# Performance work log

Measured on AMD Instinct MI355X. Metric: run time of the kernel, lower is better.

Reference implementation:

```python
import jax, jax.numpy as jnp
import numpy as np

TOP_K = 2


def setup_inputs() -> dict:
    key = jax.random.key(0)
    k0, k1, k2, k3 = jax.random.split(key, 4)
    N, D, O, E = 131072, 512, 512, 16
    H = D // 4  # gate hidden: gate_input_size // 4
    x = jax.random.normal(k0, (N, D), dtype=jnp.float32)
    # gate MLP params (task_bh=0 gate; Linear weights stored as [in, out])
    Wg1 = jax.random.normal(k1, (D, H), dtype=jnp.float32) / np.sqrt(D).astype(np.float32)
    bg1 = jnp.zeros((H,), jnp.float32)
    Wg2 = jax.random.normal(k2, (H, E), dtype=jnp.float32) * 0.02
    bg2 = jnp.zeros((E,), jnp.float32)
    # per-expert Linear(D, O) weights stacked [E, D, O]
    We = jax.random.normal(k3, (E, D, O), dtype=jnp.float32) / np.sqrt(D).astype(np.float32)
    be = jnp.zeros((E, O), jnp.float32)
    return {"x": x, "Wg1": Wg1, "bg1": bg1, "Wg2": Wg2, "bg2": bg2,
            "We": We, "be": be, "task_bh": 0}


def reference(x, Wg1, bg1, Wg2, bg2, We, be, task_bh):
    # --- top_k_gating (noisy_gating=False path) ---
    h = jax.nn.gelu(x @ Wg1 + bg1, approximate=False)  # nn.GELU default is exact erf
    logits = h @ Wg2 + bg2                              # [N, E]
    probs = jax.nn.softmax(logits, axis=1) + 1e-4       # [N, E]
    top_g, top_i = jax.lax.top_k(probs, TOP_K)          # [N, K]
    N, E = probs.shape
    # dense gate matrix: zeros.scatter(1, top_k_indices, top_k_gates)
    gates = jnp.zeros_like(probs).at[jnp.arange(N)[:, None], top_i].set(top_g)
    # --- dispatch / per-expert GEMM / combine ---
    # Equivalent to: gather tokens per expert, expert Linear, scale by gate,
    # scatter-add back. Since gates[n, e] == 0 for unselected experts, the
    # combined output equals sum_e gates[:, e] * (x @ We[e] + be[e]).
    def body(acc, ewb):
        W_e, b_e, g_e = ewb                      # [D,O], [O], [N]
        return acc + g_e[:, None] * (x @ W_e + b_e), None
    init = jnp.zeros((N, We.shape[2]), x.dtype)
    out, _ = jax.lax.scan(body, init, (We, be, gates.T))
    return out
```

## Files before the change

kernel.cpp:

```cpp
#include <hip/hip_runtime.h>
#include <cstdint>
#include <math.h>


#define NTOK 131072
#define DDIM 512
#define NT 16

typedef _Float16 f16;
typedef f16   f16x8 __attribute__((ext_vector_type(8)));
typedef float f32x4 __attribute__((ext_vector_type(4)));

__device__ __forceinline__ void load_lds16(const void* g, void* l){
  __builtin_amdgcn_global_load_lds(
      (const __attribute__((address_space(1))) void*)(uintptr_t)g,
      (__attribute__((address_space(3))) void*)(uintptr_t)l, 16, 0, 0);
}

__device__ __forceinline__ f32x4 MFMAH(f16x8 a, f16x8 b, f32x4 c){
  return __builtin_amdgcn_mfma_f32_16x16x32_f16(a, b, c, 0, 0, 0);
}

__device__ __forceinline__ f16x8 readF64h(const char* buf, int r, int q){
  return *(const f16x8*)(buf + r*128 + ((q ^ (r & 7)) << 4));
}
__device__ __forceinline__ f16x8 pack8f(const float* fv){
  f16x8 v;
  #pragma unroll
  for (int j=0;j<8;++j) v[j] = (f16)fv[j];
  return v;
}

__global__ void kconv(const float* __restrict__ We, const float* __restrict__ Wg1,
                      const float* __restrict__ Wg2,
                      f16* __restrict__ Wt, f16* __restrict__ W1, char* __restrict__ Wg2f,
                      int* __restrict__ ctrl){
  __shared__ float sh[64*65];
  int bx = blockIdx.x, tid = threadIdx.x;
  if (bx < 1024){
    int e = bx >> 6, dt = (bx >> 3) & 7, ot = bx & 7;
    const float* src = We + (size_t)e*262144 + (size_t)dt*64*512 + ot*64;
    #pragma unroll
    for (int it=0; it<16; ++it){ int idx = it*256+tid; int dl = idx>>6, ol = idx&63;
      sh[dl*65+ol] = src[dl*512+ol]; }
    __syncthreads();
    f16* dst = Wt + (size_t)e*262144 + (size_t)ot*64*512 + dt*64;
    #pragma unroll
    for (int it=0; it<16; ++it){ int idx = it*256+tid; int ol = idx>>6, dl = idx&63;
      dst[(size_t)ol*512+dl] = (f16)sh[dl*65+ol]; }
  } else if (bx < 1040){
    int q = bx - 1024;
    int dt = q >> 1, ht = q & 1;
    const float* src = Wg1 + (size_t)dt*64*128 + ht*64;
    #pragma unroll
    for (int it=0; it<16; ++it){ int idx = it*256+tid; int dl = idx>>6, ol = idx&63;
      sh[dl*65+ol] = src[dl*128+ol]; }
    __syncthreads();
    #pragma unroll
    for (int it=0; it<16; ++it){ int idx = it*256+tid; int ol = idx>>6, dl = idx&63;
      W1[(size_t)(ht*64+ol)*512 + dt*64+dl] = (f16)sh[dl*65+ol]; }
  } else {
    int ks = tid >> 6, l = tid & 63;
    int col = l & 15, kb = ks*32 + ((l >> 4) << 3);
    f16x8 v;
    #pragma unroll
    for (int j=0;j<8;++j) v[j] = (f16)Wg2[(kb+j)*16 + col];
    *(f16x8*)(Wg2f + (ks*64+l)*16) = v;
    #pragma unroll
    for (int i = 0; i < 8; ++i) ctrl[tid + i*256] = 0;
  }
}

__global__ __launch_bounds__(256) void kgate(
    const float* __restrict__ x, const f16* __restrict__ W1, const char* __restrict__ Wg2f,
    const float* __restrict__ bg1, const float* __restrict__ bg2,
    f16* __restrict__ xbf,
    int2* __restrict__ gate_e, float2* __restrict__ gate_g,
    int* __restrict__ refine_cnt, int* __restrict__ refine_list, int* __restrict__ counts)
{
  __shared__ __align__(16) char sm[76800];
  const int BOFF = 32768;
  const int LOGI = 67584;
  const int HIST = 75776;
  int tid = threadIdx.x, bid = blockIdx.x;
  int lane = tid & 63, w = tid >> 6, wm = w >> 1, wn = w & 1;
  int l15 = lane & 15, l4 = lane >> 4;
  int t0 = bid * 128;
  int ar = tid >> 1, ach = tid & 1;
  const float* xrow = x + (size_t)(t0 + ar) * DDIM;
  char* xbfb = (char*)xbf;
  f32x4 acc[4][4];
  #pragma unroll
  for (int n=0;n<4;++n){
    float bb = bg1[wn*64 + n*16 + l15];
    f32x4 z = {bb, bb, bb, bb};
    #pragma unroll
    for (int m=0;m<4;++m) acc[m][n] = z;
  }
  auto stageA = [&](int ks, char* abuf){
    float fv[32];
    #pragma unroll
    for (int q=0;q<8;++q) *(float4*)&fv[q*4] = *(const float4*)(xrow + ks*64 + ach*32 + q*4);
    f16x8 h0 = pack8f(fv), h1 = pack8f(fv+8), h2 = pack8f(fv+16), h3 = pack8f(fv+24);
    *(f16x8*)(abuf + ar*128 + (((ach*4+0) ^ (ar & 7)) << 4)) = h0;
    *(f16x8*)(abuf + ar*128 + (((ach*4+1) ^ (ar & 7)) << 4)) = h1;
    *(f16x8*)(abuf + ar*128 + (((ach*4+2) ^ (ar & 7)) << 4)) = h2;
    *(f16x8*)(abuf + ar*128 + (((ach*4+3) ^ (ar & 7)) << 4)) = h3;
    if (xbf){
      char* xd = xbfb + (size_t)(t0+ar)*1024 + ks*128 + ach*64;
      *(f16x8*)xd = h0; *(f16x8*)(xd+16) = h1; *(f16x8*)(xd+32) = h2; *(f16x8*)(xd+48) = h3;
    }
  };
  auto stageB = [&](int ks, char* lds){
    const char* gb = (const char*)W1 + ks*128;
    #pragma unroll
    for (int i = 0; i < 4; ++i){
      int lin = i*4096 + tid*16;
      int r = lin >> 7, g = (lin >> 4) & 7;
      load_lds16(gb + r*1024 + ((g ^ (r & 7)) << 4), lds + i*4096 + ((tid >> 6) << 10));
    }
  };
  stageB(0, sm + BOFF); stageA(0, sm);
  for (int ks = 0; ks < 8; ++ks){
    int b = ks & 1;
    asm volatile("s_waitcnt vmcnt(0)" ::: "memory");
    __syncthreads();
    if (ks < 7) stageB(ks+1, sm + BOFF + (b^1)*16384);
    const char* Ab = sm + b*16384;
    const char* Bb = sm + BOFF + b*16384;
    f16x8 ah[4][2], bh[4][2];
    #pragma unroll
    for (int m=0;m<4;++m)
      #pragma unroll
      for (int kf=0;kf<2;++kf) ah[m][kf] = readF64h(Ab, wm*64 + m*16 + l15, kf*4 + l4);
    #pragma unroll
    for (int n=0;n<4;++n)
      #pragma unroll
      for (int kf=0;kf<2;++kf) bh[n][kf] = readF64h(Bb, wn*64 + n*16 + l15, kf*4 + l4);
    #pragma unroll
    for (int m=0;m<4;++m)
      #pragma unroll
      for (int n=0;n<4;++n){
        acc[m][n] = MFMAH(ah[m][0], bh[n][0], acc[m][n]);
        acc[m][n] = MFMAH(ah[m][1], bh[n][1], acc[m][n]);
      }
    if (ks < 7) stageA(ks+1, sm + (b^1)*16384);
  }
  __syncthreads();
  uint4 wgf[4];
  #pragma unroll
  for (int ksq=0; ksq<4; ++ksq) wgf[ksq] = *(const uint4*)(Wg2f + (ksq*64+lane)*16);
  float* hl = (float*)sm;
  #pragma unroll
  for (int m=0;m<4;++m)
    #pragma unroll
    for (int n=0;n<4;++n)
      #pragma unroll
      for (int j=0;j<4;++j){
        int row = wm*64 + m*16 + (l4 << 2) + j;
        int col = wn*64 + n*16 + l15;
        float uv = acc[m][n][j];
        hl[row*132 + col] = 0.5f * uv * (1.0f + erff(uv * 0.70710678118654752f));
      }
  __syncthreads();
  {
    float bb2 = bg2[l15];
    float* ll = (float*)(sm + LOGI);
    #pragma unroll
    for (int sub=0; sub<2; ++sub){
      f32x4 acc2 = {bb2, bb2, bb2, bb2};
      #pragma unroll
      for (int ksq=0; ksq<4; ++ksq){
        const float* hp = (const float*)sm + (w*32 + sub*16 + l15)*132 + ksq*32 + l4*8;
        f16x8 afr;
        #pragma unroll
        for (int j=0;j<8;++j) afr[j] = (f16)hp[j];
        acc2 = MFMAH(afr, *(const f16x8*)&wgf[ksq], acc2);
      }
      #pragma unroll
      for (int j=0;j<4;++j) ll[(w*32 + sub*16 + l4*4 + j)*16 + l15] = acc2[j];
    }
  }
  int* hist = (int*)(sm + HIST);
  hist[tid] = 0;
  __syncthreads();
  if (tid < 128){
    int t = t0 + tid;
    const float* l = (const float*)(sm + LOGI) + tid*16;
    float b1 = -1e30f, b2 = -1e30f, b3 = -1e30f; int e1 = 0, e2 = 0;
    #pragma unroll
    for (int e = 0; e < 16; ++e){
      float v = l[e];
      if (v > b1){ b3 = b2; b2 = b1; e2 = e1; b1 = v; e1 = e; }
      else if (v > b2){ b3 = b2; b2 = v; e2 = e; }
      else if (v > b3){ b3 = v; }
    }
    float s = 0.f;
    #pragma unroll
    for (int e = 0; e < 16; ++e) s += expf(l[e] - b1);
    float inv = 1.f / s;
    gate_e[t] = make_int2(e1, e2);
    gate_g[t] = make_float2(inv + 1e-4f, expf(b2 - b1) * inv + 1e-4f);
    if (b2 - b3 < 1e-3f){
      int pos = atomicAdd(refine_cnt, 1);
      refine_list[pos] = t;
    }
    int pa = min(e1, e2), pb = max(e1, e2);
    atomicAdd(&hist[pa*16 + pb], 1);
  }
  __syncthreads();
  if (hist[tid]) atomicAdd(&counts[tid], hist[tid]);
}

__global__ __launch_bounds__(128) void krefine(
    const float* __restrict__ x, const float* __restrict__ Wg1, const float* __restrict__ bg1,
    const float* __restrict__ Wg2, const float* __restrict__ bg2,
    const int* __restrict__ refine_cnt, const int* __restrict__ refine_list,
    int2* __restrict__ gate_e, float2* __restrict__ gate_g, int* __restrict__ counts)
{
  __shared__ float  xs[512];
  __shared__ double hd[128];
  __shared__ double ld[16];
  int tid = threadIdx.x;
  int rc = *refine_cnt;
  for (int i = blockIdx.x; i < rc; i += gridDim.x){
    __syncthreads();
    int t = refine_list[i];
    *(float4*)(xs + tid*4) = *(const float4*)(x + (size_t)t*DDIM + tid*4);
    __syncthreads();
    double a0=0.0, a1=0.0, a2=0.0, a3=0.0;
    for (int d = 0; d < 512; d += 4){
      a0 += (double)xs[d]   * (double)Wg1[(d)*128 + tid];
      a1 += (double)xs[d+1] * (double)Wg1[(d+1)*128 + tid];
      a2 += (double)xs[d+2] * (double)Wg1[(d+2)*128 + tid];
      a3 += (double)xs[d+3] * (double)Wg1[(d+3)*128 + tid];
    }
    double a = (double)bg1[tid] + ((a0+a1)+(a2+a3));
    hd[tid] = 0.5 * a * (1.0 + erf(a * 0.70710678118654752440));
    __syncthreads();
    if (tid < 16){
      double s0=0.0, s1=0.0;
      for (int k = 0; k < 128; k += 2){
        s0 += hd[k]   * (double)Wg2[(k)*16 + tid];
        s1 += hd[k+1] * (double)Wg2[(k+1)*16 + tid];
      }
      ld[tid] = (double)bg2[tid] + s0 + s1;
    }
    __syncthreads();
    if (tid == 0){
      int2 olde = gate_e[t];
      double b1 = -1e300, b2 = -1e300; int e1 = 0, e2 = 0;
      for (int e = 0; e < 16; ++e){
        double v = ld[e];
        if (v > b1){ b2 = b1; e2 = e1; b1 = v; e1 = e; }
        else if (v > b2){ b2 = v; e2 = e; }
      }
      double s = 0.0;
      for (int e = 0; e < 16; ++e) s += exp(ld[e] - b1);
      double inv = 1.0 / s;
      int oldp = min(olde.x, olde.y)*16 + max(olde.x, olde.y);
      int newp = min(e1, e2)*16 + max(e1, e2);
      if (oldp != newp){ atomicSub(&counts[oldp], 1); atomicAdd(&counts[newp], 1); }
      gate_e[t] = make_int2(e1, e2);
      gate_g[t] = make_float2((float)(inv + 1e-4), (float)(exp(b2 - b1) * inv + 1e-4));
    }
  }
}

__global__ __launch_bounds__(256) void kscatter(
    const int2* __restrict__ gate_e, const float2* __restrict__ gate_g,
    const int* __restrict__ counts,
    int* __restrict__ bases, int* __restrict__ cursors,
    int* __restrict__ tile_pair, int* __restrict__ tile_row0, int* __restrict__ ntiles,
    int* __restrict__ pair_tok, float2* __restrict__ pair_g, int ts)
{
  __shared__ int h[256];
  __shared__ int gb[256];
  __shared__ int bl[257];
  int tid = threadIdx.x;
  h[tid] = 0;
  if (tid < 64){
    int l = tid;
    int4 c = *(const int4*)(counts + l*4);
    int s = c.x + c.y + c.z + c.w;
    int ps = s;
    #pragma unroll
    for (int d = 1; d < 64; d <<= 1){ int v = __shfl_up(ps, d); if (l >= d) ps += v; }
    int ex = ps - s;
    bl[4*l+0] = ex;
    bl[4*l+1] = ex + c.x;
    bl[4*l+2] = ex + c.x + c.y;
    bl[4*l+3] = ex + c.x + c.y + c.z;
    if (l == 63) bl[256] = ex + s;
    if (blockIdx.x == 0){
      *(int4*)(bases + 4*l) = make_int4(bl[4*l], bl[4*l+1], bl[4*l+2], bl[4*l+3]);
      if (l == 63) bases[256] = ex + s;
      int t0 = (c.x + ts-1)/ts, t1 = (c.y + ts-1)/ts, t2 = (c.z + ts-1)/ts, t3 = (c.w + ts-1)/ts;
      int tsum = t0 + t1 + t2 + t3;
      int pt = tsum;
      #pragma unroll
      for (int d = 1; d < 64; d <<= 1){ int v = __shfl_up(pt, d); if (l >= d) pt += v; }
      int ext = pt - tsum;
      if (l == 63) *ntiles = ext + tsum;
      int tb = ext;
      int cc[4] = {c.x, c.y, c.z, c.w};
      #pragma unroll
      for (int j = 0; j < 4; ++j){
        int pp = 4*l + j;
        for (int r = 0; r < cc[j]; r += ts){ tile_pair[tb] = pp; tile_row0[tb] = r; ++tb; }
      }
    }
  }
  __syncthreads();
  int t = blockIdx.x*256 + tid;
  int2 ee = gate_e[t]; float2 gg = gate_g[t];
  int a, b; float ga, gbv;
  if (ee.x < ee.y){ a = ee.x; b = ee.y; ga = gg.x; gbv = gg.y; }
  else            { a = ee.y; b = ee.x; ga = gg.y; gbv = gg.x; }
  int p = a*16 + b;
  int off = atomicAdd(&h[p], 1);
  __syncthreads();
  if (h[tid]) gb[tid] = bl[tid] + atomicAdd(&cursors[tid], h[tid]);
  __syncthreads();
  int slot = gb[p] + off;
  pair_tok[slot] = t;
  pair_g[slot] = make_float2(ga, gbv);
}

#define SB0 __builtin_amdgcn_sched_barrier(0)
#define PH_MID do{ __builtin_amdgcn_s_barrier(); \
                   asm volatile("s_waitcnt lgkmcnt(0)"); SB0; }while(0)
#define PH_END do{ SB0; __builtin_amdgcn_s_barrier(); }while(0)

#define RDA(hp, mb) do{ \
  _Pragma("unroll") for (int m_=0;m_<4;++m_){ \
    int r_ = ((mb)+m_)*16 + l15; \
    af[m_][0] = readF64h(hp, r_, l4); \
    af[m_][1] = readF64h(hp, r_, 4+l4); }}while(0)
#define RDB(hp, bv, nb) do{ \
  _Pragma("unroll") for (int n_=0;n_<2;++n_){ \
    int r_ = bln + ((nb)+n_)*16 + l15; \
    bv[n_][0] = readF64h(hp, r_, l4); \
    bv[n_][1] = readF64h(hp, r_, 4+l4); }}while(0)
#define MMAC(bv, mb, nb) do{ \
  __builtin_amdgcn_s_setprio(1); \
  _Pragma("unroll") for (int m_=0;m_<4;++m_){ \
    _Pragma("unroll") for (int n_=0;n_<2;++n_){ \
      acc[(mb)+m_][(nb)+n_] = MFMAH(af[m_][0], bv[n_][0], acc[(mb)+m_][(nb)+n_]); \
      acc[(mb)+m_][(nb)+n_] = MFMAH(af[m_][1], bv[n_][1], acc[(mb)+m_][(nb)+n_]); }} \
  __builtin_amdgcn_s_setprio(0); \
}while(0)

__global__ __launch_bounds__(512, 2) void kexpert2(
    const f16* __restrict__ xbf, const f16* __restrict__ Wt, const float* __restrict__ be,
    float* __restrict__ out,
    const int* __restrict__ counts, const int* __restrict__ bases,
    const int* __restrict__ tile_pair, const int* __restrict__ tile_row0, const int* __restrict__ ntiles,
    const int* __restrict__ pair_tok, const float2* __restrict__ pair_g)
{
  __shared__ __align__(16) char sm[134144];
  const int BBASE = 65536, LTOK = 131072, LG = 132096;
  int bid = blockIdx.x;
  int tile = ((bid >> 4) << 3) | (bid & 7);
  int nt = (bid >> 3) & 1;
  if (tile >= *ntiles) return;
  int p = tile_pair[tile], row0 = tile_row0[tile];
  int base = bases[p], cnt = counts[p];
  int eA = p >> 4, eB = p & 15;
  int tid = threadIdx.x, lane = tid & 63, w = tid >> 6;
  int wm = w >> 2, wn = w & 3;
  int l15 = lane & 15, l4 = lane >> 4;
  int bln = (wn & 1) * 64;
  if (tid < 256){
    int rr = row0 + tid; bool v = rr < cnt;
    ((int*)(sm + LTOK))[tid] = v ? pair_tok[base + rr] : -1;
    ((float2*)(sm + LG))[tid] = v ? pair_g[base + rr] : make_float2(0.f, 1.f);
  }
  __syncthreads();

  int rr0 = tid >> 3;
  int sw = ((tid & 7) ^ (rr0 & 7)) << 4;
  const char* xb = (const char*)xbf;
  const char* srcA[2][2];
  #pragma unroll
  for (int h = 0; h < 2; ++h)
    #pragma unroll
    for (int i = 0; i < 2; ++i){
      int tk = ((const int*)(sm + LTOK))[h*128 + i*64 + rr0];
      if (tk < 0) tk = 0;
      srcA[h][i] = xb + (size_t)tk*1024 + sw;
    }
  const char* srcB0 = (const char*)Wt + (size_t)eA*524288 + (size_t)(nt*256 + rr0)*1024 + sw;
  long long edelt = ((long long)eB - eA) * 524288;
  char* dA = sm + w*1024;
  char* dB = sm + BBASE + w*1024;

  auto stA = [&](int t, int h){
    if (t >= NT) return;
    int ks = t & 7, bf_ = t & 1;
    load_lds16(srcA[h][0] + ks*128, dA + bf_*32768 + h*16384);
    load_lds16(srcA[h][1] + ks*128, dA + bf_*32768 + h*16384 + 8192);
  };
  auto stB = [&](int t, int h){
    if (t >= NT) return;
    int ks = t & 7, bf_ = t & 1;
    long long eo = ((t >= 8) ? edelt : 0) + ks*128;
    load_lds16(srcB0 + h*131072 + eo,         dB + bf_*32768 + h*16384);
    load_lds16(srcB0 + h*131072 + 65536 + eo, dB + bf_*32768 + h*16384 + 8192);
  };

  const char* A0 = sm + wm*16384;
  const char* A1 = A0 + 32768;
  const char* B0 = sm + BBASE + (wn >> 1)*16384;
  const char* B1 = B0 + 32768;

  f32x4 acc[8][4];
  #pragma unroll
  for (int m = 0; m < 8; ++m)
    #pragma unroll
    for (int n = 0; n < 4; ++n) acc[m][n] = (f32x4){0.f,0.f,0.f,0.f};

  stA(0,0); stA(0,1); stB(0,0); stB(0,1); stB(1,0); stB(1,1);
  asm volatile("s_waitcnt vmcnt(4)"); SB0;
  __builtin_amdgcn_s_barrier();

  f16x8 af[4][2], bL[2][2], bH[2][2];
  #pragma unroll 1
  for (int i = 0; i < 8; ++i){
    int t0 = 2*i, t1 = t0 + 1;
    RDA(A0, 0); RDB(B0, bL, 0); stA(t1, 0);
    PH_MID; MMAC(bL, 0, 0); PH_END;
    RDB(B0, bH, 2); stA(t1, 1);
    PH_MID; MMAC(bH, 0, 2); PH_END;
    RDA(A0, 4); stB(t0+2, 0);
    PH_MID; MMAC(bH, 4, 2); PH_END;
    stB(t0+2, 1);
    if (i != 7) { asm volatile("s_waitcnt vmcnt(4)"); SB0; }
    else        { asm volatile("s_waitcnt vmcnt(0)"); SB0; }
    PH_MID; MMAC(bL, 4, 0); PH_END;
    RDA(A1, 0); RDB(B1, bL, 0); stA(t0+2, 0);
    PH_MID; MMAC(bL, 0, 0); PH_END;
    RDB(B1, bH, 2); stA(t0+2, 1);
    PH_MID; MMAC(bH, 0, 2); PH_END;
    RDA(A1, 4); stB(t1+2, 0);
    PH_MID; MMAC(bH, 4, 2); PH_END;
    stB(t1+2, 1);
    if (i != 7) { asm volatile("s_waitcnt vmcnt(4)"); SB0; }
    PH_MID; MMAC(bL, 4, 0); PH_END;
    if (i == 3){
      #pragma unroll
      for (int m = 0; m < 8; ++m)
        #pragma unroll
        for (int j = 0; j < 4; ++j){
          int row = wm*128 + m*16 + l4*4 + j;
          float2 g2 = ((const float2*)(sm + LG))[row];
          float r_ = g2.x / g2.y;
          #pragma unroll
          for (int n = 0; n < 4; ++n) acc[m][n][j] *= r_;
        }
    }
  }

  float bcA[4], bcB[4];
  #pragma unroll
  for (int n = 0; n < 4; ++n){
    int col = nt*256 + wn*64 + n*16 + l15;
    bcA[n] = be[(size_t)eA*DDIM + col];
    bcB[n] = be[(size_t)eB*DDIM + col];
  }
  #pragma unroll
  for (int m = 0; m < 8; ++m)
    #pragma unroll
    for (int j = 0; j < 4; ++j){
      int row = wm*128 + m*16 + l4*4 + j;
      int tk = ((const int*)(sm + LTOK))[row];
      if (tk >= 0){
        float2 g2 = ((const float2*)(sm + LG))[row];
        float* orow = out + (size_t)tk*DDIM + nt*256 + wn*64;
        #pragma unroll
        for (int n = 0; n < 4; ++n)
          orow[n*16 + l15] = g2.y*acc[m][n][j] + g2.x*bcA[n] + g2.y*bcB[n];
      }
    }
}

__global__ __launch_bounds__(256, 2) void kexpertF(
    const float* __restrict__ x,
    const f16* __restrict__ Wt, const float* __restrict__ be,
    float* __restrict__ out,
    const int* __restrict__ counts, const int* __restrict__ bases,
    const int* __restrict__ tile_pair, const int* __restrict__ tile_row0, const int* __restrict__ ntiles,
    const int* __restrict__ pair_tok, const float2* __restrict__ pair_g)
{
  __shared__ __align__(16) char sm[67072];
  const int ABUF = 0, BBUF = 32768, LTOK = 65536, LGOFF = 66048;
  int tile = blockIdx.x >> 2, nt = blockIdx.x & 3;
  if (tile >= *ntiles) return;
  int p = tile_pair[tile], row0 = tile_row0[tile];
  int base = bases[p], cnt = counts[p];
  int eA = p >> 4, eB = p & 15;
  int tid = threadIdx.x, lane = tid & 63;
  int w = tid >> 6, wm = w >> 1, wn = w & 1;
  if (tid < 128){
    int rr = row0 + tid; bool v = rr < cnt;
    ((int*)(sm + LTOK))[tid] = v ? pair_tok[base + rr] : -1;
    ((float2*)(sm + LGOFF))[tid] = v ? pair_g[base + rr] : make_float2(0.f, 0.f);
  }
  __syncthreads();
  const char* wb = (const char*)Wt;
  int grp = tid >> 3, gch = tid & 7;
  int swz = (gch ^ (grp & 7)) << 4;
  long long edelt = ((long long)eB - (long long)eA) * 524288;
  const char* srcB[4];
  #pragma unroll
  for (int i = 0; i < 4; ++i)
    srcB[i] = wb + (long long)eA*524288 + (size_t)(nt*128 + i*32 + grp)*1024 + swz;
  int arow = tid >> 1, ach = tid & 1;
  int tkr = ((const int*)(sm + LTOK))[arow];
  if (tkr < 0) tkr = 0;
  const float* xrow = x + (size_t)tkr*DDIM + ach*32;
  int ldst = (w << 10);
  #pragma unroll
  for (int i = 0; i < 4; ++i) load_lds16(srcB[i], sm + BBUF + i*4096 + ldst);
  {
    #pragma unroll
    for (int q2 = 0; q2 < 4; ++q2){
      float fv[8];
      *(float4*)&fv[0] = *(const float4*)(xrow + q2*8);
      *(float4*)&fv[4] = *(const float4*)(xrow + q2*8 + 4);
      f16x8 hv = pack8f(fv);
      int g = ach*4 + q2;
      *(f16x8*)(sm + ABUF + arow*128 + ((g ^ (arow & 7)) << 4)) = hv;
    }
  }
  f32x4 acc[4][4], res[4][4];
  #pragma unroll
  for (int m=0;m<4;++m)
    #pragma unroll
    for (int n=0;n<4;++n) acc[m][n] = (f32x4){0.f,0.f,0.f,0.f};
  for (int u = 0; u < 16; ++u){
    int b = u & 1;
    asm volatile("s_waitcnt vmcnt(0)" ::: "memory");
    __syncthreads();
    int un = u + 1;
    f16x8 hv[4];
    if (un < 16){
      int b2 = un & 1;
      long long aoff = (long long)(un & 7) * 128;
      long long boff = aoff + ((un >> 3) ? edelt : 0);
      #pragma unroll
      for (int i = 0; i < 4; ++i)
        load_lds16(srcB[i] + boff, sm + BBUF + b2*16384 + i*4096 + ldst);
      const float* xr = xrow + (un & 7)*64;
      #pragma unroll
      for (int q2 = 0; q2 < 4; ++q2){
        float fv[8];
        *(float4*)&fv[0] = *(const float4*)(xr + q2*8);
        *(float4*)&fv[4] = *(const float4*)(xr + q2*8 + 4);
        hv[q2] = pack8f(fv);
      }
    }
    const char* Ab = sm + ABUF + b*16384;
    const char* Bb = sm + BBUF + b*16384;
    f16x8 af2[4][2], bf2[4][2];
    #pragma unroll
    for (int m=0;m<4;++m){
      int r = wm*64 + m*16 + (lane & 15);
      af2[m][0] = readF64h(Ab, r, (lane >> 4));
      af2[m][1] = readF64h(Ab, r, 4 + (lane >> 4));
    }
    #pragma unroll
    for (int n=0;n<4;++n){
      int r = wn*64 + n*16 + (lane & 15);
      bf2[n][0] = readF64h(Bb, r, (lane >> 4));
      bf2[n][1] = readF64h(Bb, r, 4 + (lane >> 4));
    }
    #pragma unroll
    for (int m=0;m<4;++m)
      #pragma unroll
      for (int n=0;n<4;++n){
        acc[m][n] = MFMAH(af2[m][0], bf2[n][0], acc[m][n]);
        acc[m][n] = MFMAH(af2[m][1], bf2[n][1], acc[m][n]);
      }
    if (un < 16){
      int b2 = un & 1;
      #pragma unroll
      for (int q2 = 0; q2 < 4; ++q2){
        int g = ach*4 + q2;
        *(f16x8*)(sm + ABUF + b2*16384 + arow*128 + ((g ^ (arow & 7)) << 4)) = hv[q2];
      }
    }
    if (u == 7){
      const float* bev = be + (size_t)eA*DDIM + nt*128;
      float bcol[4];
      #pragma unroll
      for (int n=0;n<4;++n) bcol[n] = bev[wn*64 + n*16 + (lane & 15)];
      #pragma unroll
      for (int m=0;m<4;++m)
        #pragma unroll
        for (int j=0;j<4;++j){
          int row = wm*64 + m*16 + ((lane >> 4) << 2) + j;
          float g = ((const float2*)(sm + LGOFF))[row].x;
          #pragma unroll
          for (int n=0;n<4;++n){
            res[m][n][j] = g * (acc[m][n][j] + bcol[n]);
            acc[m][n][j] = 0.f;
          }
        }
    }
    if (u == 15){
      const float* bev = be + (size_t)eB*DDIM + nt*128;
      float bcol[4];
      #pragma unroll
      for (int n=0;n<4;++n) bcol[n] = bev[wn*64 + n*16 + (lane & 15)];
      #pragma unroll
      for (int m=0;m<4;++m)
        #pragma unroll
        for (int j=0;j<4;++j){
          int row = wm*64 + m*16 + ((lane >> 4) << 2) + j;
          int tk = ((const int*)(sm + LTOK))[row];
          float g = ((const float2*)(sm + LGOFF))[row].y;
          if (tk >= 0){
            float* orow = out + (size_t)tk*DDIM + nt*128;
            #pragma unroll
            for (int n=0;n<4;++n)
              orow[wn*64 + n*16 + (lane & 15)] = res[m][n][j] + g * (acc[m][n][j] + bcol[n]);
          }
        }
    }
  }
}

extern "C" void kernel_launch(void* const* d_in, const int* in_sizes, int n_in,
                              void* d_out, int out_size, void* d_ws, size_t ws_size,
                              hipStream_t stream)
{
  const float* x   = (const float*)d_in[0];
  const float* Wg1 = (const float*)d_in[1];
  const float* bg1 = (const float*)d_in[2];
  const float* Wg2 = (const float*)d_in[3];
  const float* bg2 = (const float*)d_in[4];
  const float* We  = (const float*)d_in[5];
  const float* be  = (const float*)d_in[6];
  float* out = (float*)d_out;
  char* ws = (char*)d_ws;

  f16*  Wt          = (f16*)(ws + 0);
  f16*  W1          = (f16*)(ws + 8388608);
  char* Wg2f        = ws + 8519680;
  char* CTRL        = ws + 8650752;
  int*  refine_cnt  = (int*)(CTRL);
  int*  ntiles      = (int*)(CTRL + 4);
  int*  counts      = (int*)(CTRL + 64);
  int*  cursors     = (int*)(CTRL + 2048);
  int*  bases       = (int*)(CTRL + 4096);
  int2*   gate_e    = (int2*)(ws + 8658944);
  float2* gate_g    = (float2*)(ws + 9707520);
  int*  refine_list = (int*)(ws + 10756096);
  int*  pair_tok    = (int*)(ws + 11280384);
  float2* pair_g    = (float2*)(ws + 11804672);
  int*  tile_pair   = (int*)(ws + 12853248);
  int*  tile_row0   = (int*)(ws + 12863488);
  const size_t XBF_OFF = 16777216ull;
  const size_t XBF_BYTES = (size_t)NTOK * DDIM * 2;
  bool bf16a = ws_size >= XBF_OFF + XBF_BYTES;
  f16* xbf = bf16a ? (f16*)(ws + XBF_OFF) : nullptr;

  hipLaunchKernelGGL(kconv,    dim3(1041), dim3(256), 0, stream, We, Wg1, Wg2, Wt, W1, Wg2f,
                     (int*)CTRL);
  hipLaunchKernelGGL(kgate,    dim3(1024), dim3(256), 0, stream, x, W1, Wg2f, bg1, bg2,
                     xbf, gate_e, gate_g, refine_cnt, refine_list, counts);
  hipLaunchKernelGGL(krefine,  dim3(512),  dim3(128), 0, stream, x, Wg1, bg1, Wg2, bg2,
                     refine_cnt, refine_list, gate_e, gate_g, counts);
  hipLaunchKernelGGL(kscatter, dim3(512),  dim3(256), 0, stream, gate_e, gate_g, counts,
                     bases, cursors, tile_pair, tile_row0, ntiles, pair_tok, pair_g,
                     bf16a ? 256 : 128);
  if (bf16a)
    hipLaunchKernelGGL(kexpert2, dim3(1408), dim3(512), 0, stream, xbf, Wt, be, out,
                       counts, bases, tile_pair, tile_row0, ntiles, pair_tok, pair_g);
  else
    hipLaunchKernelGGL(kexpertF, dim3(5120), dim3(256), 0, stream, x, Wt, be, out,
                       counts, bases, tile_pair, tile_row0, ntiles, pair_tok, pair_g);
  (void)in_sizes; (void)n_in; (void)out_size; (void)ws_size;
}
```

Measured before the change: 461.0 us.

## Fold expert weight transpose into gate kernel and widen MFMA phases

The fp32-to-fp16 transpose of the expert weights moves out of the conversion kernel and into the tail of the gate kernel, one 64x64 tile per gate block. This shrinks the conversion launch to 17 blocks and lets the transpose run alongside gate work. The expert GEMM main loop also reads all four B fragments at once and issues 32 MFMAs per phase instead of 16, halving the barrier-delimited phases. The cost is more live fragment registers and coarser interleaving of global loads with MFMAs.

```diff
diff --git a/kernel.cpp b/kernel.cpp
--- a/kernel.cpp
+++ b/kernel.cpp
@@ -31,26 +31,12 @@
   return v;
 }
 
-__global__ void kconv(const float* __restrict__ We, const float* __restrict__ Wg1,
-                      const float* __restrict__ Wg2,
-                      f16* __restrict__ Wt, f16* __restrict__ W1, char* __restrict__ Wg2f,
-                      int* __restrict__ ctrl){
+__global__ void kconv(const float* __restrict__ Wg1, const float* __restrict__ Wg2,
+                      f16* __restrict__ W1, char* __restrict__ Wg2f, int* __restrict__ ctrl){
   __shared__ float sh[64*65];
   int bx = blockIdx.x, tid = threadIdx.x;
-  if (bx < 1024){
-    int e = bx >> 6, dt = (bx >> 3) & 7, ot = bx & 7;
-    const float* src = We + (size_t)e*262144 + (size_t)dt*64*512 + ot*64;
-    #pragma unroll
-    for (int it=0; it<16; ++it){ int idx = it*256+tid; int dl = idx>>6, ol = idx&63;
-      sh[dl*65+ol] = src[dl*512+ol]; }
-    __syncthreads();
-    f16* dst = Wt + (size_t)e*262144 + (size_t)ot*64*512 + dt*64;
-    #pragma unroll
-    for (int it=0; it<16; ++it){ int idx = it*256+tid; int ol = idx>>6, dl = idx&63;
-      dst[(size_t)ol*512+dl] = (f16)sh[dl*65+ol]; }
-  } else if (bx < 1040){
-    int q = bx - 1024;
-    int dt = q >> 1, ht = q & 1;
+  if (bx < 16){
+    int dt = bx >> 1, ht = bx & 1;
     const float* src = Wg1 + (size_t)dt*64*128 + ht*64;
     #pragma unroll
     for (int it=0; it<16; ++it){ int idx = it*256+tid; int dl = idx>>6, ol = idx&63;
@@ -74,6 +60,7 @@
 __global__ __launch_bounds__(256) void kgate(
     const float* __restrict__ x, const f16* __restrict__ W1, const char* __restrict__ Wg2f,
     const float* __restrict__ bg1, const float* __restrict__ bg2,
+    const float* __restrict__ We, f16* __restrict__ Wt,
     f16* __restrict__ xbf,
     int2* __restrict__ gate_e, float2* __restrict__ gate_g,
     int* __restrict__ refine_cnt, int* __restrict__ refine_list, int* __restrict__ counts)
@@ -210,6 +197,20 @@
   }
   __syncthreads();
   if (hist[tid]) atomicAdd(&counts[tid], hist[tid]);
+  __syncthreads();
+  {
+    float* sh = (float*)sm;
+    int e = bid >> 6, dt = (bid >> 3) & 7, ot = bid & 7;
+    const float* src = We + (size_t)e*262144 + (size_t)dt*64*512 + ot*64;
+    #pragma unroll
+    for (int it=0; it<16; ++it){ int idx = it*256+tid; int dl = idx>>6, ol = idx&63;
+      sh[dl*65+ol] = src[dl*512+ol]; }
+    __syncthreads();
+    f16* dst = Wt + (size_t)e*262144 + (size_t)ot*64*512 + dt*64;
+    #pragma unroll
+    for (int it=0; it<16; ++it){ int idx = it*256+tid; int ol = idx>>6, dl = idx&63;
+      dst[(size_t)ol*512+dl] = (f16)sh[dl*65+ol]; }
+  }
 }
 
 __global__ __launch_bounds__(128) void krefine(
@@ -337,17 +338,17 @@
     int r_ = ((mb)+m_)*16 + l15; \
     af[m_][0] = readF64h(hp, r_, l4); \
     af[m_][1] = readF64h(hp, r_, 4+l4); }}while(0)
-#define RDB(hp, bv, nb) do{ \
-  _Pragma("unroll") for (int n_=0;n_<2;++n_){ \
-    int r_ = bln + ((nb)+n_)*16 + l15; \
-    bv[n_][0] = readF64h(hp, r_, l4); \
-    bv[n_][1] = readF64h(hp, r_, 4+l4); }}while(0)
-#define MMAC(bv, mb, nb) do{ \
+#define RDB4(hp) do{ \
+  _Pragma("unroll") for (int n_=0;n_<4;++n_){ \
+    int r_ = bln + n_*16 + l15; \
+    bb[n_][0] = readF64h(hp, r_, l4); \
+    bb[n_][1] = readF64h(hp, r_, 4+l4); }}while(0)
+#define MMAC32(mb) do{ \
   __builtin_amdgcn_s_setprio(1); \
   _Pragma("unroll") for (int m_=0;m_<4;++m_){ \
-    _Pragma("unroll") for (int n_=0;n_<2;++n_){ \
-      acc[(mb)+m_][(nb)+n_] = MFMAH(af[m_][0], bv[n_][0], acc[(mb)+m_][(nb)+n_]); \
-      acc[(mb)+m_][(nb)+n_] = MFMAH(af[m_][1], bv[n_][1], acc[(mb)+m_][(nb)+n_]); }} \
+    _Pragma("unroll") for (int n_=0;n_<4;++n_){ \
+      acc[(mb)+m_][n_] = MFMAH(af[m_][0], bb[n_][0], acc[(mb)+m_][n_]); \
+      acc[(mb)+m_][n_] = MFMAH(af[m_][1], bb[n_][1], acc[(mb)+m_][n_]); }} \
   __builtin_amdgcn_s_setprio(0); \
 }while(0)
 
@@ -424,29 +425,21 @@
   asm volatile("s_waitcnt vmcnt(4)"); SB0;
   __builtin_amdgcn_s_barrier();
 
-  f16x8 af[4][2], bL[2][2], bH[2][2];
+  f16x8 af[4][2], bb[4][2];
   #pragma unroll 1
   for (int i = 0; i < 8; ++i){
     int t0 = 2*i, t1 = t0 + 1;
-    RDA(A0, 0); RDB(B0, bL, 0); stA(t1, 0);
-    PH_MID; MMAC(bL, 0, 0); PH_END;
-    RDB(B0, bH, 2); stA(t1, 1);
-    PH_MID; MMAC(bH, 0, 2); PH_END;
-    RDA(A0, 4); stB(t0+2, 0);
-    PH_MID; MMAC(bH, 4, 2); PH_END;
-    stB(t0+2, 1);
+    RDA(A0, 0); RDB4(B0); stA(t1, 0); stA(t1, 1);
+    PH_MID; MMAC32(0); PH_END;
+    RDA(A0, 4); stB(t0+2, 0); stB(t0+2, 1);
     if (i != 7) { asm volatile("s_waitcnt vmcnt(4)"); SB0; }
     else        { asm volatile("s_waitcnt vmcnt(0)"); SB0; }
-    PH_MID; MMAC(bL, 4, 0); PH_END;
-    RDA(A1, 0); RDB(B1, bL, 0); stA(t0+2, 0);
-    PH_MID; MMAC(bL, 0, 0); PH_END;
-    RDB(B1, bH, 2); stA(t0+2, 1);
-    PH_MID; MMAC(bH, 0, 2); PH_END;
-    RDA(A1, 4); stB(t1+2, 0);
-    PH_MID; MMAC(bH, 4, 2); PH_END;
-    stB(t1+2, 1);
+    PH_MID; MMAC32(4); PH_END;
+    RDA(A1, 0); RDB4(B1); stA(t0+2, 0); stA(t0+2, 1);
+    PH_MID; MMAC32(0); PH_END;
+    RDA(A1, 4); stB(t1+2, 0); stB(t1+2, 1);
     if (i != 7) { asm volatile("s_waitcnt vmcnt(4)"); SB0; }
-    PH_MID; MMAC(bL, 4, 0); PH_END;
+    PH_MID; MMAC32(4); PH_END;
     if (i == 3){
       #pragma unroll
       for (int m = 0; m < 8; ++m)
@@ -666,10 +659,10 @@
   bool bf16a = ws_size >= XBF_OFF + XBF_BYTES;
   f16* xbf = bf16a ? (f16*)(ws + XBF_OFF) : nullptr;
 
-  hipLaunchKernelGGL(kconv,    dim3(1041), dim3(256), 0, stream, We, Wg1, Wg2, Wt, W1, Wg2f,
+  hipLaunchKernelGGL(kconv,    dim3(17),   dim3(256), 0, stream, Wg1, Wg2, W1, Wg2f,
                      (int*)CTRL);
   hipLaunchKernelGGL(kgate,    dim3(1024), dim3(256), 0, stream, x, W1, Wg2f, bg1, bg2,
-                     xbf, gate_e, gate_g, refine_cnt, refine_list, counts);
+                     We, Wt, xbf, gate_e, gate_g, refine_cnt, refine_list, counts);
   hipLaunchKernelGGL(krefine,  dim3(512),  dim3(128), 0, stream, x, Wg1, bg1, Wg2, bg2,
                      refine_cnt, refine_list, gate_e, gate_g, counts);
   hipLaunchKernelGGL(kscatter, dim3(512),  dim3(256), 0, stream, gate_e, gate_g, counts,
```

Measured after the change: 461.2 us. No clear change (+0.1%).
